# Kernel optimization log

Hardware: AMD Instinct MI355X
Metric: run time of the kernel (lower is better)

## Reference

```python
import jax, jax.numpy as jnp
import numpy as np

DIM = 256
H = 4
D = DIM // H  # head_dim = 64
SCALE = D ** -0.5


def setup_inputs() -> dict:
    key = jax.random.key(0)
    ks = jax.random.split(key, 12)
    B, N, M = 4, 2048, 2048
    x_query = jax.random.normal(ks[0], (B, N, DIM), dtype=jnp.float32)
    x_context = jax.random.normal(ks[1], (B, M, DIM), dtype=jnp.float32)
    geo_bias = jax.random.normal(ks[2], (B, H, N, M), dtype=jnp.float32)
    init = 1.0 / np.sqrt(DIM)
    Wq = jax.random.uniform(ks[3], (DIM, DIM), jnp.float32, -init, init)
    bq = jax.random.uniform(ks[4], (DIM,), jnp.float32, -init, init)
    Wk = jax.random.uniform(ks[5], (DIM, DIM), jnp.float32, -init, init)
    bk = jax.random.uniform(ks[6], (DIM,), jnp.float32, -init, init)
    Wv = jax.random.uniform(ks[7], (DIM, DIM), jnp.float32, -init, init)
    bv = jax.random.uniform(ks[8], (DIM,), jnp.float32, -init, init)
    Wo = jax.random.uniform(ks[9], (DIM, DIM), jnp.float32, -init, init)
    bo = jax.random.uniform(ks[10], (DIM,), jnp.float32, -init, init)
    return {"x_query": x_query, "x_context": x_context, "geo_bias": geo_bias,
            "Wq": Wq, "bq": bq, "Wk": Wk, "bk": bk, "Wv": Wv, "bv": bv,
            "Wo": Wo, "bo": bo}


def reference(x_query, x_context, geo_bias, Wq, bq, Wk, bk, Wv, bv, Wo, bo):
    B, N, _ = x_query.shape
    M = x_context.shape[1]
    # projections; nn.Linear computes x @ W.T + b
    q = (x_query @ Wq.T + bq).reshape(B, N, H, D).transpose(0, 2, 1, 3)   # (B,H,N,D)
    k = (x_context @ Wk.T + bk).reshape(B, M, H, D).transpose(0, 2, 1, 3)  # (B,H,M,D)
    v = (x_context @ Wv.T + bv).reshape(B, M, H, D).transpose(0, 2, 1, 3)  # (B,H,M,D)
    attn = jnp.einsum("bhnd,bhmd->bhnm", q, k) * SCALE + geo_bias
    attn = jax.nn.softmax(attn, axis=-1)
    out = jnp.einsum("bhnm,bhmd->bhnd", attn, v)
    out = out.transpose(0, 2, 1, 3).reshape(B, N, DIM)
    return out @ Wo.T + bo
```

## Files before the change

kernel.cpp:

```cpp
#include <hip/hip_runtime.h>

typedef unsigned short u16;
typedef unsigned int u32;
using bf16x8  = __attribute__((ext_vector_type(8))) __bf16;
using u16x8   = __attribute__((ext_vector_type(8), may_alias)) u16;
using u16x4   = __attribute__((ext_vector_type(4), may_alias)) u16;
using f32x4   = __attribute__((ext_vector_type(4))) float;
using f32x4_a = __attribute__((ext_vector_type(4), may_alias)) float;

#define DEV __device__ __forceinline__

constexpr int Bn = 4, Hn = 4, Nn = 2048, Mn = 2048, Dn = 64, DIMn = 256;
constexpr float SCALEc = 0.125f;
constexpr float SHIFTc = 12.0f;
constexpr int LSTRIDE = 152;

DEV float bf2f(u16 h) { u32 u = ((u32)h) << 16; return __builtin_bit_cast(float, u); }
DEV u16 f2bf(float f) {
    u32 u = __builtin_bit_cast(u32, f);
    u += 0x7fffu + ((u >> 16) & 1u);
    return (u16)(u >> 16);
}
DEV bf16x8 ld8bf(const u16* p) {
    return __builtin_bit_cast(bf16x8, *reinterpret_cast<const u16x8*>(p));
}
DEV bf16x8 ld8f_bf(const float* p) {
    const f32x4 a = *reinterpret_cast<const f32x4_a*>(p);
    const f32x4 b = *reinterpret_cast<const f32x4_a*>(p + 4);
    u16x8 r;
    r[0] = f2bf(a[0]); r[1] = f2bf(a[1]); r[2] = f2bf(a[2]); r[3] = f2bf(a[3]);
    r[4] = f2bf(b[0]); r[5] = f2bf(b[1]); r[6] = f2bf(b[2]); r[7] = f2bf(b[3]);
    return __builtin_bit_cast(bf16x8, r);
}

__global__ __launch_bounds__(256) void qproj_kernel(
    const float* __restrict__ X, const float* __restrict__ W,
    const float* __restrict__ bias, float* __restrict__ Q)
{
    const int row0 = blockIdx.x * 32;
    const int wave = threadIdx.x >> 6, lane = threadIdx.x & 63;
    const int quad = lane >> 4, l16 = lane & 15;
    const int o0 = wave * 64;
    const int b = row0 >> 11, n0 = row0 & 2047;

    f32x4 acc[2][4] = {};
    #pragma unroll
    for (int k0 = 0; k0 < 256; k0 += 32) {
        bf16x8 af[2], wf[4];
        #pragma unroll
        for (int ns = 0; ns < 2; ns++)
            af[ns] = ld8f_bf(X + (size_t)(row0 + ns * 16 + l16) * DIMn + k0 + quad * 8);
        #pragma unroll
        for (int os = 0; os < 4; os++)
            wf[os] = ld8f_bf(W + (size_t)(o0 + os * 16 + l16) * DIMn + k0 + quad * 8);
        #pragma unroll
        for (int ns = 0; ns < 2; ns++)
            #pragma unroll
            for (int os = 0; os < 4; os++)
                acc[ns][os] = __builtin_amdgcn_mfma_f32_16x16x32_bf16(af[ns], wf[os], acc[ns][os], 0, 0, 0);
    }
    #pragma unroll
    for (int os = 0; os < 4; os++) {
        const int col = o0 + os * 16 + l16;
        const int h = col >> 6, d = col & 63;
        const float bb = bias[col];
        #pragma unroll
        for (int ns = 0; ns < 2; ns++)
            #pragma unroll
            for (int r = 0; r < 4; r++) {
                const int n = n0 + ns * 16 + quad * 4 + r;
                Q[((size_t)(b * Hn + h) * Nn + n) * Dn + d] = acc[ns][os][r] + bb;
            }
    }
}

__global__ __launch_bounds__(256) void kvproj_kernel(
    const float* __restrict__ X,
    const float* __restrict__ Wk, const float* __restrict__ bk,
    const float* __restrict__ Wv, const float* __restrict__ bv,
    u16* __restrict__ K, u16* __restrict__ V)
{
    const int row0 = blockIdx.x * 32;
    const int wave = threadIdx.x >> 6, lane = threadIdx.x & 63;
    const int quad = lane >> 4, l16 = lane & 15;
    const int o0 = wave * 64;
    const int b = row0 >> 11, n0 = row0 & 2047;

    f32x4 ack[2][4] = {};
    f32x4 acv[4][2] = {};
    #pragma unroll
    for (int k0 = 0; k0 < 256; k0 += 32) {
        bf16x8 af[2], wkf[4], wvf[4];
        #pragma unroll
        for (int ns = 0; ns < 2; ns++)
            af[ns] = ld8f_bf(X + (size_t)(row0 + ns * 16 + l16) * DIMn + k0 + quad * 8);
        #pragma unroll
        for (int os = 0; os < 4; os++) {
            wkf[os] = ld8f_bf(Wk + (size_t)(o0 + os * 16 + l16) * DIMn + k0 + quad * 8);
            wvf[os] = ld8f_bf(Wv + (size_t)(o0 + os * 16 + l16) * DIMn + k0 + quad * 8);
        }
        #pragma unroll
        for (int ns = 0; ns < 2; ns++)
            #pragma unroll
            for (int os = 0; os < 4; os++) {
                ack[ns][os] = __builtin_amdgcn_mfma_f32_16x16x32_bf16(af[ns], wkf[os], ack[ns][os], 0, 0, 0);
                acv[os][ns] = __builtin_amdgcn_mfma_f32_16x16x32_bf16(wvf[os], af[ns], acv[os][ns], 0, 0, 0);
            }
    }
    #pragma unroll
    for (int os = 0; os < 4; os++) {
        const int col = o0 + os * 16 + l16;
        const int h = col >> 6, d = col & 63;
        const float bb = bk[col];
        #pragma unroll
        for (int ns = 0; ns < 2; ns++)
            #pragma unroll
            for (int r = 0; r < 4; r++) {
                const int m = n0 + ns * 16 + quad * 4 + r;
                K[((size_t)(b * Hn + h) * Mn + m) * Dn + d] = f2bf(ack[ns][os][r] + bb);
            }
    }
    #pragma unroll
    for (int os = 0; os < 4; os++)
        #pragma unroll
        for (int r = 0; r < 4; r++) {
            const int colf = o0 + os * 16 + quad * 4 + r;
            const int h = colf >> 6, d = colf & 63;
            const float bb = bv[colf];
            #pragma unroll
            for (int ns = 0; ns < 2; ns++) {
                const int m = n0 + ns * 16 + l16;
                V[((size_t)(b * Hn + h) * Dn + d) * Mn + m] = f2bf(acv[os][ns][r] + bb);
            }
        }
}

__global__ __launch_bounds__(256) void attn_kernel(
    const float* __restrict__ Q,
    const u16* __restrict__ K,
    const u16* __restrict__ V,
    const float* __restrict__ geo,
    float* __restrict__ Pnum,
    float* __restrict__ Lsum,
    int S)
{
    __shared__ __align__(16) u16 lds[4][16 * LSTRIDE];

    const int h = blockIdx.y;
    const int b = blockIdx.z / S, split = blockIdx.z % S;
    const int wave = threadIdx.x >> 6, lane = threadIdx.x & 63;
    const int quad = lane >> 4, l16 = lane & 15;
    const int nbase = blockIdx.x * 64 + wave * 16;
    const int mlen = Mn / S, mbeg = split * mlen;

    const float* Qh = Q + ((size_t)(b * Hn + h) * Nn + nbase) * Dn;
    const u16*   Kh = K + (size_t)(b * Hn + h) * Mn * Dn;
    const u16*   Vh = V + (size_t)(b * Hn + h) * Dn * Mn;
    const float* Gl = geo + ((size_t)(b * Hn + h) * Nn + nbase + l16) * (size_t)Mn;

    bf16x8 qh[2], ql[2];
    #pragma unroll
    for (int kh = 0; kh < 2; kh++) {
        const float* qp = Qh + (size_t)l16 * Dn + kh * 32 + quad * 8;
        const f32x4 a = *reinterpret_cast<const f32x4_a*>(qp);
        const f32x4 c = *reinterpret_cast<const f32x4_a*>(qp + 4);
        u16x8 hi, lo;
        #pragma unroll
        for (int j = 0; j < 4; j++) {
            hi[j] = f2bf(a[j]); lo[j] = f2bf(a[j] - bf2f(hi[j]));
            hi[4 + j] = f2bf(c[j]); lo[4 + j] = f2bf(c[j] - bf2f(hi[4 + j]));
        }
        qh[kh] = __builtin_bit_cast(bf16x8, hi);
        ql[kh] = __builtin_bit_cast(bf16x8, lo);
    }

    f32x4 oacc[4] = {};
    float lsum = 0.f;
    u16* pl = &lds[wave][0];

    for (int m0 = mbeg; m0 < mbeg + mlen; m0 += 128) {
        #pragma unroll
        for (int ms = 0; ms < 8; ms++) {
            const int mb = m0 + ms * 16;
            const u16* kp = Kh + (size_t)(mb + l16) * Dn + quad * 8;
            const bf16x8 kb0 = ld8bf(kp);
            const bf16x8 kb1 = ld8bf(kp + 32);
            f32x4 s = {};
            s = __builtin_amdgcn_mfma_f32_16x16x32_bf16(kb0, qh[0], s, 0, 0, 0);
            s = __builtin_amdgcn_mfma_f32_16x16x32_bf16(kb0, ql[0], s, 0, 0, 0);
            s = __builtin_amdgcn_mfma_f32_16x16x32_bf16(kb1, qh[1], s, 0, 0, 0);
            s = __builtin_amdgcn_mfma_f32_16x16x32_bf16(kb1, ql[1], s, 0, 0, 0);
            const f32x4 g = *reinterpret_cast<const f32x4_a*>(Gl + mb + quad * 4);
            u16x4 pk;
            float ls = 0.f;
            #pragma unroll
            for (int r = 0; r < 4; r++) {
                const float p = __expf(fmaf(s[r], SCALEc, g[r]) - SHIFTc);
                ls += p;
                pk[r] = f2bf(p);
            }
            lsum += ls;
            *reinterpret_cast<u16x4*>(pl + l16 * LSTRIDE + ms * 16 + quad * 4) = pk;
        }
        #pragma unroll
        for (int kh = 0; kh < 4; kh++) {
            const bf16x8 pa = ld8bf(pl + l16 * LSTRIDE + kh * 32 + quad * 8);
            #pragma unroll
            for (int ds = 0; ds < 4; ds++) {
                const bf16x8 vb = ld8bf(Vh + (size_t)(ds * 16 + l16) * Mn + (m0 - mbeg) + mbeg + kh * 32 + quad * 8);
                oacc[ds] = __builtin_amdgcn_mfma_f32_16x16x32_bf16(pa, vb, oacc[ds], 0, 0, 0);
            }
        }
    }

    lsum += __shfl_xor(lsum, 16);
    lsum += __shfl_xor(lsum, 32);

    float* PN = Pnum + (size_t)split * (Bn * (size_t)Nn * DIMn)
                     + ((size_t)b * Nn + nbase) * DIMn + h * Dn;
    #pragma unroll
    for (int r = 0; r < 4; r++)
        #pragma unroll
        for (int ds = 0; ds < 4; ds++)
            PN[(size_t)(quad * 4 + r) * DIMn + ds * 16 + l16] = oacc[ds][r];

    if (lane < 16)
        Lsum[(((size_t)split * Bn + b) * Hn + h) * Nn + nbase + l16] = lsum;
}

__global__ __launch_bounds__(256) void combine_kernel(
    const float* __restrict__ Pnum, const float* __restrict__ Lsum,
    u16* __restrict__ AO, int S)
{
    const int idx = blockIdx.x * 256 + threadIdx.x;
    const int row = idx >> 5;
    const int c0  = (idx & 31) * 8;
    const int b = row >> 11, n = row & 2047, h = c0 >> 6;

    float l = 0.f;
    for (int s = 0; s < S; s++)
        l += Lsum[(((size_t)s * Bn + b) * Hn + h) * Nn + n];
    const float inv = 1.0f / l;

    f32x4 a0 = {}, a1 = {};
    for (int s = 0; s < S; s++) {
        const float* p = Pnum + (size_t)s * (Bn * (size_t)Nn * DIMn) + (size_t)row * DIMn + c0;
        a0 += *reinterpret_cast<const f32x4_a*>(p);
        a1 += *reinterpret_cast<const f32x4_a*>(p + 4);
    }
    u16x8 o;
    #pragma unroll
    for (int j = 0; j < 4; j++) {
        o[j]     = f2bf(a0[j] * inv);
        o[4 + j] = f2bf(a1[j] * inv);
    }
    *reinterpret_cast<u16x8*>(AO + (size_t)row * DIMn + c0) = o;
}

__global__ __launch_bounds__(256) void oproj_kernel(
    const u16* __restrict__ A, const float* __restrict__ W,
    const float* __restrict__ bias, float* __restrict__ out)
{
    const int row0 = blockIdx.x * 32;
    const int wave = threadIdx.x >> 6, lane = threadIdx.x & 63;
    const int quad = lane >> 4, l16 = lane & 15;
    const int o0 = wave * 64;

    f32x4 acc[2][4] = {};
    #pragma unroll
    for (int k0 = 0; k0 < 256; k0 += 32) {
        bf16x8 af[2], wf[4];
        #pragma unroll
        for (int ns = 0; ns < 2; ns++)
            af[ns] = ld8bf(A + (size_t)(row0 + ns * 16 + l16) * DIMn + k0 + quad * 8);
        #pragma unroll
        for (int os = 0; os < 4; os++)
            wf[os] = ld8f_bf(W + (size_t)(o0 + os * 16 + l16) * DIMn + k0 + quad * 8);
        #pragma unroll
        for (int ns = 0; ns < 2; ns++)
            #pragma unroll
            for (int os = 0; os < 4; os++)
                acc[ns][os] = __builtin_amdgcn_mfma_f32_16x16x32_bf16(af[ns], wf[os], acc[ns][os], 0, 0, 0);
    }
    #pragma unroll
    for (int os = 0; os < 4; os++) {
        const int col = o0 + os * 16 + l16;
        const float bb = bias[col];
        #pragma unroll
        for (int ns = 0; ns < 2; ns++)
            #pragma unroll
            for (int r = 0; r < 4; r++) {
                const int row = row0 + ns * 16 + quad * 4 + r;
                out[(size_t)row * DIMn + col] = acc[ns][os][r] + bb;
            }
    }
}

extern "C" void kernel_launch(void* const* d_in, const int* in_sizes, int n_in,
                              void* d_out, int out_size, void* d_ws, size_t ws_size,
                              hipStream_t stream) {
    const float* xq  = (const float*)d_in[0];
    const float* xc  = (const float*)d_in[1];
    const float* geo = (const float*)d_in[2];
    const float* Wq  = (const float*)d_in[3];
    const float* bq  = (const float*)d_in[4];
    const float* Wk  = (const float*)d_in[5];
    const float* bk  = (const float*)d_in[6];
    const float* Wv  = (const float*)d_in[7];
    const float* bv  = (const float*)d_in[8];
    const float* Wo  = (const float*)d_in[9];
    const float* bo  = (const float*)d_in[10];

    const int S = (ws_size >= (60ull << 20)) ? 4 : 1;

    char* ws = (char*)d_ws;
    float* Qw   = (float*)ws;
    u16*   Kw   = (u16*)(ws + (8ull << 20));
    u16*   Vw   = (u16*)(ws + (12ull << 20));
    u16*   AOw  = (u16*)(ws + (16ull << 20));
    float* Pnum = (float*)(ws + (20ull << 20));
    float* Lsum = (float*)(ws + (20ull << 20) + (size_t)S * (8ull << 20));

    qproj_kernel<<<256, 256, 0, stream>>>(xq, Wq, bq, Qw);
    kvproj_kernel<<<256, 256, 0, stream>>>(xc, Wk, bk, Wv, bv, Kw, Vw);
    attn_kernel<<<dim3(Nn / 64, Hn, Bn * S), 256, 0, stream>>>(Qw, Kw, Vw, geo, Pnum, Lsum, S);
    combine_kernel<<<(Bn * Nn * 32) / 256, 256, 0, stream>>>(Pnum, Lsum, AOw, S);
    oproj_kernel<<<256, 256, 0, stream>>>(AOw, Wo, bo, (float*)d_out);
}
```

Measured before the change: 557.7 us.

## Fuse QKV projections, double attention row tile, prefetch K/geo, shrink GEMM tiles

```diff
diff --git a/kernel.cpp b/kernel.cpp
--- a/kernel.cpp
+++ b/kernel.cpp
@@ -33,109 +33,87 @@
     return __builtin_bit_cast(bf16x8, r);
 }
 
-__global__ __launch_bounds__(256) void qproj_kernel(
-    const float* __restrict__ X, const float* __restrict__ W,
-    const float* __restrict__ bias, float* __restrict__ Q)
+__global__ __launch_bounds__(256, 4) void qkv_kernel(
+    const float* __restrict__ Xq, const float* __restrict__ Wq, const float* __restrict__ bq,
+    const float* __restrict__ Xc, const float* __restrict__ Wk, const float* __restrict__ bk,
+    const float* __restrict__ Wv, const float* __restrict__ bv,
+    float* __restrict__ Q, u16* __restrict__ K, u16* __restrict__ V)
 {
-    const int row0 = blockIdx.x * 32;
     const int wave = threadIdx.x >> 6, lane = threadIdx.x & 63;
     const int quad = lane >> 4, l16 = lane & 15;
     const int o0 = wave * 64;
-    const int b = row0 >> 11, n0 = row0 & 2047;
-
-    f32x4 acc[2][4] = {};
-    #pragma unroll
-    for (int k0 = 0; k0 < 256; k0 += 32) {
-        bf16x8 af[2], wf[4];
-        #pragma unroll
-        for (int ns = 0; ns < 2; ns++)
-            af[ns] = ld8f_bf(X + (size_t)(row0 + ns * 16 + l16) * DIMn + k0 + quad * 8);
+
+    if (blockIdx.x < 512) {
+        const int row0 = blockIdx.x * 16;
+        const int b = row0 >> 11, n0 = row0 & 2047;
+        f32x4 acc[4] = {};
+        #pragma unroll
+        for (int k0 = 0; k0 < 256; k0 += 32) {
+            bf16x8 wf[4];
+            const bf16x8 af = ld8f_bf(Xq + (size_t)(row0 + l16) * DIMn + k0 + quad * 8);
+            #pragma unroll
+            for (int os = 0; os < 4; os++)
+                wf[os] = ld8f_bf(Wq + (size_t)(o0 + os * 16 + l16) * DIMn + k0 + quad * 8);
+            #pragma unroll
+            for (int os = 0; os < 4; os++)
+                acc[os] = __builtin_amdgcn_mfma_f32_16x16x32_bf16(af, wf[os], acc[os], 0, 0, 0);
+        }
+        #pragma unroll
+        for (int os = 0; os < 4; os++) {
+            const int col = o0 + os * 16 + l16;
+            const int h = col >> 6, d = col & 63;
+            const float bb = bq[col];
+            #pragma unroll
+            for (int r = 0; r < 4; r++) {
+                const int n = n0 + quad * 4 + r;
+                Q[((size_t)(b * Hn + h) * Nn + n) * Dn + d] = acc[os][r] + bb;
+            }
+        }
+    } else {
+        const int row0 = (blockIdx.x - 512) * 16;
+        const int b = row0 >> 11, n0 = row0 & 2047;
+        f32x4 ack[4] = {};
+        f32x4 acv[4] = {};
+        #pragma unroll
+        for (int k0 = 0; k0 < 256; k0 += 32) {
+            bf16x8 wkf[4], wvf[4];
+            const bf16x8 af = ld8f_bf(Xc + (size_t)(row0 + l16) * DIMn + k0 + quad * 8);
+            #pragma unroll
+            for (int os = 0; os < 4; os++) {
+                wkf[os] = ld8f_bf(Wk + (size_t)(o0 + os * 16 + l16) * DIMn + k0 + quad * 8);
+                wvf[os] = ld8f_bf(Wv + (size_t)(o0 + os * 16 + l16) * DIMn + k0 + quad * 8);
+            }
+            #pragma unroll
+            for (int os = 0; os < 4; os++) {
+                ack[os] = __builtin_amdgcn_mfma_f32_16x16x32_bf16(af, wkf[os], ack[os], 0, 0, 0);
+                acv[os] = __builtin_amdgcn_mfma_f32_16x16x32_bf16(wvf[os], af, acv[os], 0, 0, 0);
+            }
+        }
+        #pragma unroll
+        for (int os = 0; os < 4; os++) {
+            const int col = o0 + os * 16 + l16;
+            const int h = col >> 6, d = col & 63;
+            const float bb = bk[col];
+            #pragma unroll
+            for (int r = 0; r < 4; r++) {
+                const int m = n0 + quad * 4 + r;
+                K[((size_t)(b * Hn + h) * Mn + m) * Dn + d] = f2bf(ack[os][r] + bb);
+            }
+        }
         #pragma unroll
         for (int os = 0; os < 4; os++)
-            wf[os] = ld8f_bf(W + (size_t)(o0 + os * 16 + l16) * DIMn + k0 + quad * 8);
-        #pragma unroll
-        for (int ns = 0; ns < 2; ns++)
-            #pragma unroll
-            for (int os = 0; os < 4; os++)
-                acc[ns][os] = __builtin_amdgcn_mfma_f32_16x16x32_bf16(af[ns], wf[os], acc[ns][os], 0, 0, 0);
-    }
-    #pragma unroll
-    for (int os = 0; os < 4; os++) {
-        const int col = o0 + os * 16 + l16;
-        const int h = col >> 6, d = col & 63;
-        const float bb = bias[col];
-        #pragma unroll
-        for (int ns = 0; ns < 2; ns++)
             #pragma unroll
             for (int r = 0; r < 4; r++) {
-                const int n = n0 + ns * 16 + quad * 4 + r;
-                Q[((size_t)(b * Hn + h) * Nn + n) * Dn + d] = acc[ns][os][r] + bb;
-            }
-    }
-}
-
-__global__ __launch_bounds__(256) void kvproj_kernel(
-    const float* __restrict__ X,
-    const float* __restrict__ Wk, const float* __restrict__ bk,
-    const float* __restrict__ Wv, const float* __restrict__ bv,
-    u16* __restrict__ K, u16* __restrict__ V)
-{
-    const int row0 = blockIdx.x * 32;
-    const int wave = threadIdx.x >> 6, lane = threadIdx.x & 63;
-    const int quad = lane >> 4, l16 = lane & 15;
-    const int o0 = wave * 64;
-    const int b = row0 >> 11, n0 = row0 & 2047;
-
-    f32x4 ack[2][4] = {};
-    f32x4 acv[4][2] = {};
-    #pragma unroll
-    for (int k0 = 0; k0 < 256; k0 += 32) {
-        bf16x8 af[2], wkf[4], wvf[4];
-        #pragma unroll
-        for (int ns = 0; ns < 2; ns++)
-            af[ns] = ld8f_bf(X + (size_t)(row0 + ns * 16 + l16) * DIMn + k0 + quad * 8);
-        #pragma unroll
-        for (int os = 0; os < 4; os++) {
-            wkf[os] = ld8f_bf(Wk + (size_t)(o0 + os * 16 + l16) * DIMn + k0 + quad * 8);
-            wvf[os] = ld8f_bf(Wv + (size_t)(o0 + os * 16 + l16) * DIMn + k0 + quad * 8);
-        }
-        #pragma unroll
-        for (int ns = 0; ns < 2; ns++)
-            #pragma unroll
-            for (int os = 0; os < 4; os++) {
-                ack[ns][os] = __builtin_amdgcn_mfma_f32_16x16x32_bf16(af[ns], wkf[os], ack[ns][os], 0, 0, 0);
-                acv[os][ns] = __builtin_amdgcn_mfma_f32_16x16x32_bf16(wvf[os], af[ns], acv[os][ns], 0, 0, 0);
-            }
-    }
-    #pragma unroll
-    for (int os = 0; os < 4; os++) {
-        const int col = o0 + os * 16 + l16;
-        const int h = col >> 6, d = col & 63;
-        const float bb = bk[col];
-        #pragma unroll
-        for (int ns = 0; ns < 2; ns++)
-            #pragma unroll
-            for (int r = 0; r < 4; r++) {
-                const int m = n0 + ns * 16 + quad * 4 + r;
-                K[((size_t)(b * Hn + h) * Mn + m) * Dn + d] = f2bf(ack[ns][os][r] + bb);
-            }
-    }
-    #pragma unroll
-    for (int os = 0; os < 4; os++)
-        #pragma unroll
-        for (int r = 0; r < 4; r++) {
-            const int colf = o0 + os * 16 + quad * 4 + r;
-            const int h = colf >> 6, d = colf & 63;
-            const float bb = bv[colf];
-            #pragma unroll
-            for (int ns = 0; ns < 2; ns++) {
-                const int m = n0 + ns * 16 + l16;
-                V[((size_t)(b * Hn + h) * Dn + d) * Mn + m] = f2bf(acv[os][ns][r] + bb);
-            }
-        }
-}
-
-__global__ __launch_bounds__(256) void attn_kernel(
+                const int colf = o0 + os * 16 + quad * 4 + r;
+                const int h = colf >> 6, d = colf & 63;
+                const float bb = bv[colf];
+                const int m = n0 + l16;
+                V[((size_t)(b * Hn + h) * Dn + d) * Mn + m] = f2bf(acv[os][r] + bb);
+            }
+    }
+}
+
+__global__ __launch_bounds__(256, 4) void attn_kernel(
     const float* __restrict__ Q,
     const u16* __restrict__ K,
     const u16* __restrict__ V,
@@ -144,88 +122,122 @@
     float* __restrict__ Lsum,
     int S)
 {
-    __shared__ __align__(16) u16 lds[4][16 * LSTRIDE];
+    __shared__ __align__(16) u16 lds[4][32 * LSTRIDE];
 
     const int h = blockIdx.y;
     const int b = blockIdx.z / S, split = blockIdx.z % S;
     const int wave = threadIdx.x >> 6, lane = threadIdx.x & 63;
     const int quad = lane >> 4, l16 = lane & 15;
-    const int nbase = blockIdx.x * 64 + wave * 16;
+    const int nbase = blockIdx.x * 128 + wave * 32;
     const int mlen = Mn / S, mbeg = split * mlen;
 
     const float* Qh = Q + ((size_t)(b * Hn + h) * Nn + nbase) * Dn;
     const u16*   Kh = K + (size_t)(b * Hn + h) * Mn * Dn;
     const u16*   Vh = V + (size_t)(b * Hn + h) * Dn * Mn;
-    const float* Gl = geo + ((size_t)(b * Hn + h) * Nn + nbase + l16) * (size_t)Mn;
-
-    bf16x8 qh[2], ql[2];
-    #pragma unroll
-    for (int kh = 0; kh < 2; kh++) {
-        const float* qp = Qh + (size_t)l16 * Dn + kh * 32 + quad * 8;
-        const f32x4 a = *reinterpret_cast<const f32x4_a*>(qp);
-        const f32x4 c = *reinterpret_cast<const f32x4_a*>(qp + 4);
-        u16x8 hi, lo;
-        #pragma unroll
-        for (int j = 0; j < 4; j++) {
-            hi[j] = f2bf(a[j]); lo[j] = f2bf(a[j] - bf2f(hi[j]));
-            hi[4 + j] = f2bf(c[j]); lo[4 + j] = f2bf(c[j] - bf2f(hi[4 + j]));
-        }
-        qh[kh] = __builtin_bit_cast(bf16x8, hi);
-        ql[kh] = __builtin_bit_cast(bf16x8, lo);
-    }
-
-    f32x4 oacc[4] = {};
-    float lsum = 0.f;
+    const float* Gq0 = geo + ((size_t)(b * Hn + h) * Nn + nbase + l16) * (size_t)Mn + quad * 4;
+    const float* Gq1 = Gq0 + (size_t)16 * Mn;
+
+    bf16x8 qh[2][2], ql[2][2];
+    #pragma unroll
+    for (int nt = 0; nt < 2; nt++)
+        #pragma unroll
+        for (int kh = 0; kh < 2; kh++) {
+            const float* qp = Qh + (size_t)(nt * 16 + l16) * Dn + kh * 32 + quad * 8;
+            const f32x4 a = *reinterpret_cast<const f32x4_a*>(qp);
+            const f32x4 c = *reinterpret_cast<const f32x4_a*>(qp + 4);
+            u16x8 hi, lo;
+            #pragma unroll
+            for (int j = 0; j < 4; j++) {
+                hi[j] = f2bf(a[j]); lo[j] = f2bf(a[j] - bf2f(hi[j]));
+                hi[4 + j] = f2bf(c[j]); lo[4 + j] = f2bf(c[j] - bf2f(hi[4 + j]));
+            }
+            qh[nt][kh] = __builtin_bit_cast(bf16x8, hi);
+            ql[nt][kh] = __builtin_bit_cast(bf16x8, lo);
+        }
+
+    f32x4 oacc[2][4] = {};
+    float lsum0 = 0.f, lsum1 = 0.f;
     u16* pl = &lds[wave][0];
+    const u16* kbase = Kh + (size_t)l16 * Dn + quad * 8;
 
     for (int m0 = mbeg; m0 < mbeg + mlen; m0 += 128) {
+        const u16* kp0 = kbase + (size_t)m0 * Dn;
+        bf16x8 kb0 = ld8bf(kp0), kb1 = ld8bf(kp0 + 32);
+        f32x4 g0 = *reinterpret_cast<const f32x4_a*>(Gq0 + m0);
+        f32x4 g1 = *reinterpret_cast<const f32x4_a*>(Gq1 + m0);
         #pragma unroll
         for (int ms = 0; ms < 8; ms++) {
-            const int mb = m0 + ms * 16;
-            const u16* kp = Kh + (size_t)(mb + l16) * Dn + quad * 8;
-            const bf16x8 kb0 = ld8bf(kp);
-            const bf16x8 kb1 = ld8bf(kp + 32);
-            f32x4 s = {};
-            s = __builtin_amdgcn_mfma_f32_16x16x32_bf16(kb0, qh[0], s, 0, 0, 0);
-            s = __builtin_amdgcn_mfma_f32_16x16x32_bf16(kb0, ql[0], s, 0, 0, 0);
-            s = __builtin_amdgcn_mfma_f32_16x16x32_bf16(kb1, qh[1], s, 0, 0, 0);
-            s = __builtin_amdgcn_mfma_f32_16x16x32_bf16(kb1, ql[1], s, 0, 0, 0);
-            const f32x4 g = *reinterpret_cast<const f32x4_a*>(Gl + mb + quad * 4);
-            u16x4 pk;
-            float ls = 0.f;
+            bf16x8 nk0, nk1; f32x4 ng0, ng1;
+            if (ms < 7) {
+                const int mb = m0 + (ms + 1) * 16;
+                const u16* kp = kbase + (size_t)mb * Dn;
+                nk0 = ld8bf(kp); nk1 = ld8bf(kp + 32);
+                ng0 = *reinterpret_cast<const f32x4_a*>(Gq0 + mb);
+                ng1 = *reinterpret_cast<const f32x4_a*>(Gq1 + mb);
+            }
+            f32x4 s0 = {}, s1 = {};
+            __builtin_amdgcn_s_setprio(1);
+            s0 = __builtin_amdgcn_mfma_f32_16x16x32_bf16(kb0, qh[0][0], s0, 0, 0, 0);
+            s1 = __builtin_amdgcn_mfma_f32_16x16x32_bf16(kb0, qh[1][0], s1, 0, 0, 0);
+            s0 = __builtin_amdgcn_mfma_f32_16x16x32_bf16(kb0, ql[0][0], s0, 0, 0, 0);
+            s1 = __builtin_amdgcn_mfma_f32_16x16x32_bf16(kb0, ql[1][0], s1, 0, 0, 0);
+            s0 = __builtin_amdgcn_mfma_f32_16x16x32_bf16(kb1, qh[0][1], s0, 0, 0, 0);
+            s1 = __builtin_amdgcn_mfma_f32_16x16x32_bf16(kb1, qh[1][1], s1, 0, 0, 0);
+            s0 = __builtin_amdgcn_mfma_f32_16x16x32_bf16(kb1, ql[0][1], s0, 0, 0, 0);
+            s1 = __builtin_amdgcn_mfma_f32_16x16x32_bf16(kb1, ql[1][1], s1, 0, 0, 0);
+            __builtin_amdgcn_s_setprio(0);
+            u16x4 pk0, pk1;
+            float ls0 = 0.f, ls1 = 0.f;
             #pragma unroll
             for (int r = 0; r < 4; r++) {
-                const float p = __expf(fmaf(s[r], SCALEc, g[r]) - SHIFTc);
-                ls += p;
-                pk[r] = f2bf(p);
-            }
-            lsum += ls;
-            *reinterpret_cast<u16x4*>(pl + l16 * LSTRIDE + ms * 16 + quad * 4) = pk;
-        }
+                const float p0 = __expf(fmaf(s0[r], SCALEc, g0[r]) - SHIFTc);
+                const float p1 = __expf(fmaf(s1[r], SCALEc, g1[r]) - SHIFTc);
+                ls0 += p0; ls1 += p1;
+                pk0[r] = f2bf(p0); pk1[r] = f2bf(p1);
+            }
+            lsum0 += ls0; lsum1 += ls1;
+            *reinterpret_cast<u16x4*>(pl + l16 * LSTRIDE + ms * 16 + quad * 4) = pk0;
+            *reinterpret_cast<u16x4*>(pl + (16 + l16) * LSTRIDE + ms * 16 + quad * 4) = pk1;
+            if (ms < 7) { kb0 = nk0; kb1 = nk1; g0 = ng0; g1 = ng1; }
+        }
+        const u16* vb0 = Vh + (size_t)l16 * Mn + m0 + quad * 8;
         #pragma unroll
         for (int kh = 0; kh < 4; kh++) {
-            const bf16x8 pa = ld8bf(pl + l16 * LSTRIDE + kh * 32 + quad * 8);
+            const bf16x8 pa0 = ld8bf(pl + l16 * LSTRIDE + kh * 32 + quad * 8);
+            const bf16x8 pa1 = ld8bf(pl + (16 + l16) * LSTRIDE + kh * 32 + quad * 8);
+            bf16x8 vb[4];
+            #pragma unroll
+            for (int ds = 0; ds < 4; ds++)
+                vb[ds] = ld8bf(vb0 + (size_t)(ds * 16) * Mn + kh * 32);
+            __builtin_amdgcn_s_setprio(1);
             #pragma unroll
             for (int ds = 0; ds < 4; ds++) {
-                const bf16x8 vb = ld8bf(Vh + (size_t)(ds * 16 + l16) * Mn + (m0 - mbeg) + mbeg + kh * 32 + quad * 8);
-                oacc[ds] = __builtin_amdgcn_mfma_f32_16x16x32_bf16(pa, vb, oacc[ds], 0, 0, 0);
-            }
-        }
-    }
-
-    lsum += __shfl_xor(lsum, 16);
-    lsum += __shfl_xor(lsum, 32);
+                oacc[0][ds] = __builtin_amdgcn_mfma_f32_16x16x32_bf16(pa0, vb[ds], oacc[0][ds], 0, 0, 0);
+                oacc[1][ds] = __builtin_amdgcn_mfma_f32_16x16x32_bf16(pa1, vb[ds], oacc[1][ds], 0, 0, 0);
+            }
+            __builtin_amdgcn_s_setprio(0);
+        }
+    }
+
+    lsum0 += __shfl_xor(lsum0, 16);
+    lsum0 += __shfl_xor(lsum0, 32);
+    lsum1 += __shfl_xor(lsum1, 16);
+    lsum1 += __shfl_xor(lsum1, 32);
 
     float* PN = Pnum + (size_t)split * (Bn * (size_t)Nn * DIMn)
                      + ((size_t)b * Nn + nbase) * DIMn + h * Dn;
     #pragma unroll
-    for (int r = 0; r < 4; r++)
-        #pragma unroll
-        for (int ds = 0; ds < 4; ds++)
-            PN[(size_t)(quad * 4 + r) * DIMn + ds * 16 + l16] = oacc[ds][r];
-
-    if (lane < 16)
-        Lsum[(((size_t)split * Bn + b) * Hn + h) * Nn + nbase + l16] = lsum;
+    for (int nt = 0; nt < 2; nt++)
+        #pragma unroll
+        for (int r = 0; r < 4; r++)
+            #pragma unroll
+            for (int ds = 0; ds < 4; ds++)
+                PN[(size_t)(nt * 16 + quad * 4 + r) * DIMn + ds * 16 + l16] = oacc[nt][ds][r];
+
+    if (lane < 16) {
+        Lsum[(((size_t)split * Bn + b) * Hn + h) * Nn + nbase + l16] = lsum0;
+        Lsum[(((size_t)split * Bn + b) * Hn + h) * Nn + nbase + 16 + l16] = lsum1;
+    }
 }
 
 __global__ __launch_bounds__(256) void combine_kernel(
@@ -257,42 +269,36 @@
     *reinterpret_cast<u16x8*>(AO + (size_t)row * DIMn + c0) = o;
 }
 
-__global__ __launch_bounds__(256) void oproj_kernel(
+__global__ __launch_bounds__(256, 4) void oproj_kernel(
     const u16* __restrict__ A, const float* __restrict__ W,
     const float* __restrict__ bias, float* __restrict__ out)
 {
-    const int row0 = blockIdx.x * 32;
+    const int row0 = blockIdx.x * 16;
     const int wave = threadIdx.x >> 6, lane = threadIdx.x & 63;
     const int quad = lane >> 4, l16 = lane & 15;
     const int o0 = wave * 64;
 
-    f32x4 acc[2][4] = {};
+    f32x4 acc[4] = {};
     #pragma unroll
     for (int k0 = 0; k0 < 256; k0 += 32) {
-        bf16x8 af[2], wf[4];
-        #pragma unroll
-        for (int ns = 0; ns < 2; ns++)
-            af[ns] = ld8bf(A + (size_t)(row0 + ns * 16 + l16) * DIMn + k0 + quad * 8);
+        bf16x8 wf[4];
+        const bf16x8 af = ld8bf(A + (size_t)(row0 + l16) * DIMn + k0 + quad * 8);
         #pragma unroll
         for (int os = 0; os < 4; os++)
             wf[os] = ld8f_bf(W + (size_t)(o0 + os * 16 + l16) * DIMn + k0 + quad * 8);
         #pragma unroll
-        for (int ns = 0; ns < 2; ns++)
-            #pragma unroll
-            for (int os = 0; os < 4; os++)
-                acc[ns][os] = __builtin_amdgcn_mfma_f32_16x16x32_bf16(af[ns], wf[os], acc[ns][os], 0, 0, 0);
+        for (int os = 0; os < 4; os++)
+            acc[os] = __builtin_amdgcn_mfma_f32_16x16x32_bf16(af, wf[os], acc[os], 0, 0, 0);
     }
     #pragma unroll
     for (int os = 0; os < 4; os++) {
         const int col = o0 + os * 16 + l16;
         const float bb = bias[col];
         #pragma unroll
-        for (int ns = 0; ns < 2; ns++)
-            #pragma unroll
-            for (int r = 0; r < 4; r++) {
-                const int row = row0 + ns * 16 + quad * 4 + r;
-                out[(size_t)row * DIMn + col] = acc[ns][os][r] + bb;
-            }
+        for (int r = 0; r < 4; r++) {
+            const int row = row0 + quad * 4 + r;
+            out[(size_t)row * DIMn + col] = acc[os][r] + bb;
+        }
     }
 }
 
@@ -321,9 +327,8 @@
     float* Pnum = (float*)(ws + (20ull << 20));
     float* Lsum = (float*)(ws + (20ull << 20) + (size_t)S * (8ull << 20));
 
-    qproj_kernel<<<256, 256, 0, stream>>>(xq, Wq, bq, Qw);
-    kvproj_kernel<<<256, 256, 0, stream>>>(xc, Wk, bk, Wv, bv, Kw, Vw);
-    attn_kernel<<<dim3(Nn / 64, Hn, Bn * S), 256, 0, stream>>>(Qw, Kw, Vw, geo, Pnum, Lsum, S);
+    qkv_kernel<<<1024, 256, 0, stream>>>(xq, Wq, bq, xc, Wk, bk, Wv, bv, Qw, Kw, Vw);
+    attn_kernel<<<dim3(Nn / 128, Hn, Bn * S), 256, 0, stream>>>(Qw, Kw, Vw, geo, Pnum, Lsum, S);
     combine_kernel<<<(Bn * Nn * 32) / 256, 256, 0, stream>>>(Pnum, Lsum, AOw, S);
-    oproj_kernel<<<256, 256, 0, stream>>>(AOw, Wo, bo, (float*)d_out);
-}
+    oproj_kernel<<<Bn * Nn / 16, 256, 0, stream>>>(AOw, Wo, bo, (float*)d_out);
+}
```

Result: slower. 569.4 us (+2.1%).
